# Kernel optimization log

Measured on AMD Instinct MI355X. Metric: run time of the kernel, lower is better.

Reference implementation:

```python
import jax, jax.numpy as jnp
import numpy as np

H = 200   # n_hidden
D = 24    # d_model
B = 64
T = 2048


def setup_inputs() -> dict:
    key = jax.random.key(0)
    ks = jax.random.split(key, 7)
    s_u = 1.0 / np.sqrt(H)
    s_v = 1.0 / np.sqrt(D)
    return {
        "emb": jax.random.normal(ks[0], (B, T, D), dtype=jnp.float32),
        "h_past": jax.random.normal(ks[1], (B, T, H), dtype=jnp.float32),
        "U_w": jax.random.uniform(ks[2], (4 * H, H), jnp.float32, -s_u, s_u),
        "U_b": jax.random.uniform(ks[3], (4 * H,), jnp.float32, -s_u, s_u),
        "W_w": jax.random.uniform(ks[4], (4 * H, H), jnp.float32, -s_u, s_u),
        "V_w": jax.random.uniform(ks[5], (H, D), jnp.float32, -s_v, s_v),
        "V_b": jax.random.uniform(ks[6], (H,), jnp.float32, -s_v, s_v),
        "h_0": 0.1 * jnp.ones((1, H), dtype=jnp.float32),
        "c_0": 0.1 * jnp.ones((1, H), dtype=jnp.float32),
    }


def _run(emb, h_past, U_w, U_b, W_w, V_w, V_b, h_0, c_0):
    b = emb.shape[0]
    # Precompute input-dependent parts over all timesteps (no recurrence):
    # U(x_t) for all t: [T, B, 4H]; tanh(V(e_t)) for all t: [T, B, H]
    ux = jnp.einsum('btd,gd->tbg', h_past, U_w) + U_b
    ve = jnp.tanh(jnp.einsum('btd,hd->tbh', emb, V_w) + V_b)

    h0 = jnp.broadcast_to(h_0, (b, H))
    c0 = jnp.broadcast_to(c_0, (b, H))

    Wt = W_w.T  # [H, 4H]

    def step(carry, inp):
        h, c = carry
        ux_t, v_t = inp
        gates = ux_t + h @ Wt                     # [B, 4H]
        i_t, f_t, g_t, o_t = jnp.split(gates, 4, axis=1)
        c = jax.nn.sigmoid(f_t) * c + jax.nn.sigmoid(i_t) * jnp.tanh(g_t)
        h = jax.nn.sigmoid(o_t) * jnp.tanh(c) + v_t
        return (h, c), h

    (_, _), h_all = jax.lax.scan(step, (h0, c0), (ux, ve))
    return jnp.transpose(h_all, (1, 0, 2))  # [B, T, H]


def reference(emb, h_past, U_w, U_b, W_w, V_w, V_b, h_0, c_0):
    return _run(emb, h_past, U_w, U_b, W_w, V_w, V_b, h_0, c_0)
```

## Files before the change

kernel.cpp:

```cpp
#include <hip/hip_runtime.h>

#define HH 200
#define GG 800
#define DD 24
#define BB 64
#define TT 2048
#define CH 16
#define NT 832

__device__ __forceinline__ float fsig(float x) {
    float e = __expf(-x);
    return 1.f / (1.f + e);
}
__device__ __forceinline__ float ftanh(float x) {
    float e = __expf(2.f * x);
    return 1.f - 2.f / (e + 1.f);
}

__global__ void xpose(const float* __restrict__ src, float* __restrict__ dst) {
    int idx = blockIdx.x * blockDim.x + threadIdx.x;
    if (idx < GG * HH) {
        int g = idx / HH, j = idx % HH;
        dst[(size_t)(j >> 2) * (GG * 4) + g * 4 + (j & 3)] = src[idx];
    }
}

template <bool XP>
__global__ __launch_bounds__(NT)
void lstm_kernel(const float* __restrict__ emb,
                 const float* __restrict__ h_past,
                 const float* __restrict__ U_w,
                 const float* __restrict__ U_b,
                 const float* __restrict__ W_w,
                 const float* __restrict__ V_w,
                 const float* __restrict__ V_b,
                 const float* __restrict__ h0,
                 const float* __restrict__ c0,
                 const float* __restrict__ UT,
                 const float* __restrict__ WT,
                 float* __restrict__ out)
{
    __shared__ float ux_sh[CH][GG];
    __shared__ float hp_sh[CH][HH];
    __shared__ float emb_sh[CH][DD];
    __shared__ float h_sh[HH];
    __shared__ float g_sh[GG];
    __shared__ float Vw_sh[HH][DD + 1];
    __shared__ float Vb_sh[HH];

    const int tid = threadIdx.x;
    const int b = blockIdx.x;

    for (int i = tid; i < HH * DD; i += NT) Vw_sh[i / DD][i % DD] = V_w[i];
    if (tid < HH) { Vb_sh[tid] = V_b[tid]; h_sh[tid] = h0[tid]; }
    float c = (tid < HH) ? c0[tid] : 0.f;
    const float ub = (tid < GG) ? U_b[tid] : 0.f;

    const float* hpb  = h_past + (size_t)b * TT * HH;
    const float* embb = emb    + (size_t)b * TT * DD;
    float*       outb = out    + (size_t)b * TT * HH;

    __syncthreads();

    for (int t0 = 0; t0 < TT; t0 += CH) {
        for (int i = tid; i < CH * HH; i += NT)
            (&hp_sh[0][0])[i] = hpb[(size_t)t0 * HH + i];
        for (int i = tid; i < CH * DD; i += NT)
            (&emb_sh[0][0])[i] = embb[(size_t)t0 * DD + i];
        __syncthreads();

        if (tid < GG) {
            float2 acc[CH];
            #pragma unroll
            for (int s = 0; s < CH; ++s) acc[s] = make_float2(0.f, 0.f);
            for (int j = 0; j < HH; j += 4) {
                float4 u4;
                if (XP) u4 = *(const float4*)(UT + (size_t)(j >> 2) * (GG * 4) + tid * 4);
                else    u4 = *(const float4*)(U_w + (size_t)tid * HH + j);
                #pragma unroll
                for (int s = 0; s < CH; ++s) {
                    float4 hp4 = *(const float4*)(&hp_sh[s][j]);
                    acc[s].x = fmaf(u4.x, hp4.x, acc[s].x);
                    acc[s].y = fmaf(u4.y, hp4.y, acc[s].y);
                    acc[s].x = fmaf(u4.z, hp4.z, acc[s].x);
                    acc[s].y = fmaf(u4.w, hp4.w, acc[s].y);
                }
            }
            #pragma unroll
            for (int s = 0; s < CH; ++s) ux_sh[s][tid] = acc[s].x + acc[s].y + ub;
        }
        __syncthreads();

        for (int s = 0; s < CH; ++s) {
            float ve = 0.f;
            if (tid < HH) {
                float a = Vb_sh[tid];
                #pragma unroll
                for (int d = 0; d < DD; ++d)
                    a = fmaf(emb_sh[s][d], Vw_sh[tid][d], a);
                ve = ftanh(a);
            }
            if (tid < GG) {
                float2 g2 = make_float2(0.f, 0.f);
                for (int j = 0; j < HH; j += 4) {
                    float4 w4;
                    if (XP) w4 = *(const float4*)(WT + (size_t)(j >> 2) * (GG * 4) + tid * 4);
                    else    w4 = *(const float4*)(W_w + (size_t)tid * HH + j);
                    float4 h4 = *(const float4*)(&h_sh[j]);
                    g2.x = fmaf(w4.x, h4.x, g2.x);
                    g2.y = fmaf(w4.y, h4.y, g2.y);
                    g2.x = fmaf(w4.z, h4.z, g2.x);
                    g2.y = fmaf(w4.w, h4.w, g2.y);
                }
                float gv = g2.x + g2.y + ux_sh[s][tid];
                bool isg = (tid >= 2 * HH) && (tid < 3 * HH);
                g_sh[tid] = isg ? ftanh(gv) : fsig(gv);
            }
            __syncthreads();
            if (tid < HH) {
                float ig = g_sh[tid], fg = g_sh[HH + tid];
                float zg = g_sh[2 * HH + tid], og = g_sh[3 * HH + tid];
                c = fmaf(fg, c, ig * zg);
                float h = fmaf(og, ftanh(c), ve);
                h_sh[tid] = h;
                outb[(size_t)(t0 + s) * HH + tid] = h;
            }
            __syncthreads();
        }
    }
}

extern "C" void kernel_launch(void* const* d_in, const int* in_sizes, int n_in,
                              void* d_out, int out_size, void* d_ws, size_t ws_size,
                              hipStream_t stream) {
    const float* emb    = (const float*)d_in[0];
    const float* h_past = (const float*)d_in[1];
    const float* U_w    = (const float*)d_in[2];
    const float* U_b    = (const float*)d_in[3];
    const float* W_w    = (const float*)d_in[4];
    const float* V_w    = (const float*)d_in[5];
    const float* V_b    = (const float*)d_in[6];
    const float* h0     = (const float*)d_in[7];
    const float* c0     = (const float*)d_in[8];
    float* out = (float*)d_out;

    const size_t wneed = (size_t)2 * GG * HH * sizeof(float);
    if (ws_size >= wneed) {
        float* UT = (float*)d_ws;
        float* WT = UT + (size_t)GG * HH;
        int nb = (GG * HH + 255) / 256;
        xpose<<<nb, 256, 0, stream>>>(U_w, UT);
        xpose<<<nb, 256, 0, stream>>>(W_w, WT);
        lstm_kernel<true><<<BB, NT, 0, stream>>>(emb, h_past, U_w, U_b, W_w,
                                                 V_w, V_b, h0, c0, UT, WT, out);
    } else {
        lstm_kernel<false><<<BB, NT, 0, stream>>>(emb, h_past, U_w, U_b, W_w,
                                                  V_w, V_b, h0, c0, nullptr, nullptr, out);
    }
}
```

Baseline: 13.54 ms.

## Split LSTM hidden units across 8 blocks per batch pair with atomic cross-block sync

Replaces the one-block-per-batch kernel with 256 blocks, each owning 25 hidden units (100 gate rows) for two batch rows. Each block's W slice stays resident in LDS. Blocks exchange h every step through global memory, using release/acquire atomics and a spin-wait counter. The U·h_past projection for the next chunk is spread across steps and overlapped with the wait, and input loads are double-buffered. This cuts per-step recurrent matvec latency by spreading it across more CUs and removing global W reads. The cost is a cross-block barrier every timestep, and it depends on all 256 blocks being co-resident, or the spin-wait deadlocks.

```diff
diff --git a/kernel.cpp b/kernel.cpp
--- a/kernel.cpp
+++ b/kernel.cpp
@@ -6,7 +6,17 @@
 #define BB 64
 #define TT 2048
 #define CH 16
-#define NT 832
+#define NQ 8
+#define NRG 32
+#define KD 25
+#define NT 256
+#define NCHUNK (TT / CH)
+
+typedef float f32x2 __attribute__((ext_vector_type(2)));
+typedef float f32x4 __attribute__((ext_vector_type(4)));
+
+__device__ __forceinline__ f32x2 lo4(f32x4 v) { return __builtin_shufflevector(v, v, 0, 1); }
+__device__ __forceinline__ f32x2 hi4(f32x4 v) { return __builtin_shufflevector(v, v, 2, 3); }
 
 __device__ __forceinline__ float fsig(float x) {
     float e = __expf(-x);
@@ -17,28 +27,201 @@
     return 1.f - 2.f / (e + 1.f);
 }
 
-__global__ void xpose(const float* __restrict__ src, float* __restrict__ dst) {
-    int idx = blockIdx.x * blockDim.x + threadIdx.x;
-    if (idx < GG * HH) {
-        int g = idx / HH, j = idx % HH;
-        dst[(size_t)(j >> 2) * (GG * 4) + g * 4 + (j & 3)] = src[idx];
-    }
-}
-
-template <bool XP>
-__global__ __launch_bounds__(NT)
-void lstm_kernel(const float* __restrict__ emb,
-                 const float* __restrict__ h_past,
-                 const float* __restrict__ U_w,
-                 const float* __restrict__ U_b,
-                 const float* __restrict__ W_w,
-                 const float* __restrict__ V_w,
-                 const float* __restrict__ V_b,
-                 const float* __restrict__ h0,
-                 const float* __restrict__ c0,
-                 const float* __restrict__ UT,
-                 const float* __restrict__ WT,
-                 float* __restrict__ out)
+#define WS_NEED (4096 + 2 * NRG * NQ * 2 * KD * 4)
+
+__device__ __forceinline__ int sl(int par, int rg, int q, int b, int k) {
+    return (((par * NRG + rg) * NQ + q) * 2 + b) * KD + k;
+}
+
+__global__ void init_ws(unsigned int* ws) {
+    int i = threadIdx.x + blockIdx.x * blockDim.x;
+    if (i < 1024) ws[i] = 0u;
+}
+
+__global__ __launch_bounds__(NT, 1)
+void lstm_split(const float* __restrict__ emb,
+                const float* __restrict__ h_past,
+                const float* __restrict__ U_w,
+                const float* __restrict__ U_b,
+                const float* __restrict__ W_w,
+                const float* __restrict__ V_w,
+                const float* __restrict__ V_b,
+                const float* __restrict__ h0,
+                const float* __restrict__ c0,
+                float* __restrict__ ws,
+                float* __restrict__ out)
+{
+    __shared__ f32x4 Wt4[50 * 100];
+    __shared__ float hp_sh[2][CH][2][HH];
+    __shared__ float emb_sh[2][CH][2][DD];
+    __shared__ float h_sh[2][HH];
+    __shared__ float Vw_sh[KD][DD];
+    __shared__ float Vb_sh[KD];
+    __shared__ float g_sh[100][2];
+
+    const int tid = threadIdx.x;
+    const int bid = blockIdx.x;
+    const int rg  = bid & (NRG - 1);
+    const int q   = bid >> 5;
+    const int b0  = 2 * rg;
+
+    unsigned int* cnt = (unsigned int*)ws + (size_t)rg * 32;
+    float* sdata = ws + 1024;
+
+    const bool is_gate = (tid < 200);
+    const int r = tid >> 1;
+    const int b = tid & 1;
+    int gr = 0;
+    if (is_gate) gr = (r / KD) * HH + q * KD + (r % KD);
+    const float ub = is_gate ? U_b[gr] : 0.f;
+    const f32x4* Urow = (const f32x4*)(U_w + (size_t)gr * HH);
+
+    const bool is_upd = (tid < 2 * KD);
+    const int bu = tid / KD;
+    const int ku = tid % KD;
+    float c_reg = is_upd ? c0[q * KD + ku] : 0.f;
+
+    for (int idx = tid; idx < 100 * 50; idx += NT) {
+        int rr = idx / 50, j4 = idx % 50;
+        int grr = (rr / KD) * HH + q * KD + (rr % KD);
+        Wt4[j4 * 100 + rr] = *(const f32x4*)(W_w + (size_t)grr * HH + 4 * j4);
+    }
+    for (int idx = tid; idx < KD * DD; idx += NT)
+        Vw_sh[idx / DD][idx % DD] = V_w[(q * KD + idx / DD) * DD + idx % DD];
+    if (tid < KD) Vb_sh[tid] = V_b[q * KD + tid];
+    for (int i = tid; i < 2 * HH; i += NT) h_sh[i / HH][i % HH] = h0[i % HH];
+
+    {
+        const int t0 = 0, buf = 0;
+        for (int idx = tid; idx < CH * 2 * HH; idx += NT) {
+            int s = idx / (2 * HH), rm = idx % (2 * HH), bb = rm / HH, j = rm % HH;
+            hp_sh[buf][s][bb][j] = h_past[((size_t)(b0 + bb) * TT + (t0 + s)) * HH + j];
+        }
+        for (int idx = tid; idx < CH * 2 * DD; idx += NT) {
+            int s = idx / (2 * DD), rm = idx % (2 * DD), bb = rm / DD, d = rm % DD;
+            emb_sh[buf][s][bb][d] = emb[((size_t)(b0 + bb) * TT + (t0 + s)) * DD + d];
+        }
+    }
+    __syncthreads();
+
+    f32x2 uxc[CH], uxn[CH];
+    #pragma unroll
+    for (int i = 0; i < CH; ++i) { uxc[i] = (f32x2){0.f, 0.f}; uxn[i] = (f32x2){0.f, 0.f}; }
+
+    if (is_gate) {
+        for (int ps = 0; ps < CH; ++ps) {
+            for (int j4 = ps; j4 < 50; j4 += CH) {
+                f32x4 u = Urow[j4];
+                #pragma unroll
+                for (int s = 0; s < CH; ++s) {
+                    f32x4 hp = *(const f32x4*)&hp_sh[0][s][b][4 * j4];
+                    uxn[s] += lo4(u) * lo4(hp);
+                    uxn[s] += hi4(u) * hi4(hp);
+                }
+            }
+        }
+    }
+
+    for (int t = 0; t < TT; ++t) {
+        const int s_in = t & (CH - 1);
+        const int c    = t >> 4;
+        const int cbuf = c & 1;
+        const int nbuf = cbuf ^ 1;
+        const bool has_next = (t + CH < TT);
+        const int par1 = (t + 1) & 1;
+
+        if (s_in == 0) {
+            #pragma unroll
+            for (int i = 0; i < CH; ++i) { uxc[i] = uxn[i]; uxn[i] = (f32x2){0.f, 0.f}; }
+            if (has_next) {
+                const int t0n = (c + 1) * CH;
+                for (int idx = tid; idx < CH * 2 * HH; idx += NT) {
+                    int s = idx / (2 * HH), rm = idx % (2 * HH), bb = rm / HH, j = rm % HH;
+                    hp_sh[nbuf][s][bb][j] = h_past[((size_t)(b0 + bb) * TT + (t0n + s)) * HH + j];
+                }
+                for (int idx = tid; idx < CH * 2 * DD; idx += NT) {
+                    int s = idx / (2 * DD), rm = idx % (2 * DD), bb = rm / DD, d = rm % DD;
+                    emb_sh[nbuf][s][bb][d] = emb[((size_t)(b0 + bb) * TT + (t0n + s)) * DD + d];
+                }
+            }
+            __syncthreads();
+        }
+
+        if (is_gate) {
+            f32x2 a = (f32x2){0.f, 0.f};
+            const f32x4* hrow = (const f32x4*)&h_sh[b][0];
+            #pragma unroll 10
+            for (int j4 = 0; j4 < 50; ++j4) {
+                f32x4 w = Wt4[j4 * 100 + r];
+                f32x4 h = hrow[j4];
+                a += lo4(w) * lo4(h);
+                a += hi4(w) * hi4(h);
+            }
+            float gv = a.x + a.y + uxc[0].x + uxc[0].y + ub;
+            bool isg = (r >= 2 * KD) && (r < 3 * KD);
+            float y = fsig(isg ? 2.f * gv : gv);
+            g_sh[r][b] = isg ? 2.f * y - 1.f : y;
+            #pragma unroll
+            for (int i = 0; i < CH - 1; ++i) uxc[i] = uxc[i + 1];
+        }
+        __syncthreads();
+
+        if (is_upd) {
+            float ig = g_sh[ku][bu];
+            float fg = g_sh[KD + ku][bu];
+            float zg = g_sh[2 * KD + ku][bu];
+            float og = g_sh[3 * KD + ku][bu];
+            c_reg = fmaf(fg, c_reg, ig * zg);
+            float a = Vb_sh[ku];
+            #pragma unroll
+            for (int d = 0; d < DD; ++d)
+                a = fmaf(emb_sh[cbuf][s_in][bu][d], Vw_sh[ku][d], a);
+            float h = fmaf(og, ftanh(c_reg), ftanh(a));
+            __hip_atomic_store(&sdata[sl(par1, rg, q, bu, ku)], h,
+                               __ATOMIC_RELEASE, __HIP_MEMORY_SCOPE_AGENT);
+            out[((size_t)(b0 + bu) * TT + t) * HH + q * KD + ku] = h;
+        }
+        __syncthreads();
+
+        if (tid == 0)
+            __hip_atomic_fetch_add(cnt, 1u, __ATOMIC_RELEASE, __HIP_MEMORY_SCOPE_AGENT);
+
+        if (has_next && is_gate) {
+            for (int j4 = s_in; j4 < 50; j4 += CH) {
+                f32x4 u = Urow[j4];
+                #pragma unroll
+                for (int s = 0; s < CH; ++s) {
+                    f32x4 hp = *(const f32x4*)&hp_sh[nbuf][s][b][4 * j4];
+                    uxn[s] += lo4(u) * lo4(hp);
+                    uxn[s] += hi4(u) * hi4(hp);
+                }
+            }
+        }
+
+        if (tid == 0) {
+            const unsigned tgt = 8u * (unsigned)(t + 1);
+            while (__hip_atomic_load(cnt, __ATOMIC_ACQUIRE, __HIP_MEMORY_SCOPE_AGENT) < tgt)
+                __builtin_amdgcn_s_sleep(2);
+        }
+        __syncthreads();
+
+        for (int idx = tid; idx < NQ * 2 * KD; idx += NT) {
+            int qq = idx / (2 * KD), rm = idx % (2 * KD), bb = rm / KD, k = rm % KD;
+            float v = __hip_atomic_load(&sdata[sl(par1, rg, qq, bb, k)],
+                                        __ATOMIC_RELAXED, __HIP_MEMORY_SCOPE_AGENT);
+            h_sh[bb][qq * KD + k] = v;
+        }
+        __syncthreads();
+    }
+}
+
+#define FNT 832
+__global__ __launch_bounds__(FNT)
+void lstm_fallback(const float* __restrict__ emb, const float* __restrict__ h_past,
+                   const float* __restrict__ U_w, const float* __restrict__ U_b,
+                   const float* __restrict__ W_w, const float* __restrict__ V_w,
+                   const float* __restrict__ V_b, const float* __restrict__ h0,
+                   const float* __restrict__ c0, float* __restrict__ out)
 {
     __shared__ float ux_sh[CH][GG];
     __shared__ float hp_sh[CH][HH];
@@ -49,34 +232,25 @@
     __shared__ float Vb_sh[HH];
 
     const int tid = threadIdx.x;
-    const int b = blockIdx.x;
-
-    for (int i = tid; i < HH * DD; i += NT) Vw_sh[i / DD][i % DD] = V_w[i];
+    const int bb = blockIdx.x;
+    for (int i = tid; i < HH * DD; i += FNT) Vw_sh[i / DD][i % DD] = V_w[i];
     if (tid < HH) { Vb_sh[tid] = V_b[tid]; h_sh[tid] = h0[tid]; }
     float c = (tid < HH) ? c0[tid] : 0.f;
     const float ub = (tid < GG) ? U_b[tid] : 0.f;
-
-    const float* hpb  = h_past + (size_t)b * TT * HH;
-    const float* embb = emb    + (size_t)b * TT * DD;
-    float*       outb = out    + (size_t)b * TT * HH;
-
+    const float* hpb  = h_past + (size_t)bb * TT * HH;
+    const float* embb = emb + (size_t)bb * TT * DD;
+    float* outb = out + (size_t)bb * TT * HH;
     __syncthreads();
-
     for (int t0 = 0; t0 < TT; t0 += CH) {
-        for (int i = tid; i < CH * HH; i += NT)
-            (&hp_sh[0][0])[i] = hpb[(size_t)t0 * HH + i];
-        for (int i = tid; i < CH * DD; i += NT)
-            (&emb_sh[0][0])[i] = embb[(size_t)t0 * DD + i];
-        __syncthreads();
-
+        for (int i = tid; i < CH * HH; i += FNT) (&hp_sh[0][0])[i] = hpb[(size_t)t0 * HH + i];
+        for (int i = tid; i < CH * DD; i += FNT) (&emb_sh[0][0])[i] = embb[(size_t)t0 * DD + i];
+        __syncthreads();
         if (tid < GG) {
             float2 acc[CH];
             #pragma unroll
             for (int s = 0; s < CH; ++s) acc[s] = make_float2(0.f, 0.f);
             for (int j = 0; j < HH; j += 4) {
-                float4 u4;
-                if (XP) u4 = *(const float4*)(UT + (size_t)(j >> 2) * (GG * 4) + tid * 4);
-                else    u4 = *(const float4*)(U_w + (size_t)tid * HH + j);
+                float4 u4 = *(const float4*)(U_w + (size_t)tid * HH + j);
                 #pragma unroll
                 for (int s = 0; s < CH; ++s) {
                     float4 hp4 = *(const float4*)(&hp_sh[s][j]);
@@ -90,22 +264,18 @@
             for (int s = 0; s < CH; ++s) ux_sh[s][tid] = acc[s].x + acc[s].y + ub;
         }
         __syncthreads();
-
         for (int s = 0; s < CH; ++s) {
             float ve = 0.f;
             if (tid < HH) {
                 float a = Vb_sh[tid];
                 #pragma unroll
-                for (int d = 0; d < DD; ++d)
-                    a = fmaf(emb_sh[s][d], Vw_sh[tid][d], a);
+                for (int d = 0; d < DD; ++d) a = fmaf(emb_sh[s][d], Vw_sh[tid][d], a);
                 ve = ftanh(a);
             }
             if (tid < GG) {
                 float2 g2 = make_float2(0.f, 0.f);
                 for (int j = 0; j < HH; j += 4) {
-                    float4 w4;
-                    if (XP) w4 = *(const float4*)(WT + (size_t)(j >> 2) * (GG * 4) + tid * 4);
-                    else    w4 = *(const float4*)(W_w + (size_t)tid * HH + j);
+                    float4 w4 = *(const float4*)(W_w + (size_t)tid * HH + j);
                     float4 h4 = *(const float4*)(&h_sh[j]);
                     g2.x = fmaf(w4.x, h4.x, g2.x);
                     g2.y = fmaf(w4.y, h4.y, g2.y);
@@ -144,17 +314,12 @@
     const float* c0     = (const float*)d_in[8];
     float* out = (float*)d_out;
 
-    const size_t wneed = (size_t)2 * GG * HH * sizeof(float);
-    if (ws_size >= wneed) {
-        float* UT = (float*)d_ws;
-        float* WT = UT + (size_t)GG * HH;
-        int nb = (GG * HH + 255) / 256;
-        xpose<<<nb, 256, 0, stream>>>(U_w, UT);
-        xpose<<<nb, 256, 0, stream>>>(W_w, WT);
-        lstm_kernel<true><<<BB, NT, 0, stream>>>(emb, h_past, U_w, U_b, W_w,
-                                                 V_w, V_b, h0, c0, UT, WT, out);
+    if (ws_size >= (size_t)WS_NEED) {
+        init_ws<<<4, 256, 0, stream>>>((unsigned int*)d_ws);
+        lstm_split<<<NRG * NQ, NT, 0, stream>>>(emb, h_past, U_w, U_b, W_w,
+                                                V_w, V_b, h0, c0, (float*)d_ws, out);
     } else {
-        lstm_kernel<false><<<BB, NT, 0, stream>>>(emb, h_past, U_w, U_b, W_w,
-                                                  V_w, V_b, h0, c0, nullptr, nullptr, out);
-    }
-}
+        lstm_fallback<<<BB, FNT, 0, stream>>>(emb, h_past, U_w, U_b, W_w,
+                                              V_w, V_b, h0, c0, out);
+    }
+}
```

Measured after the change: 21.18 ms. +56.4%, slower.
